# Kernel optimization log

Measured on AMD Instinct MI355X. Metric: run time of the kernel, lower is better.

The kernel has to match this reference:

```python
import jax, jax.numpy as jnp
import numpy as np

B, S, HID = 1, 2048, 4096
NH, NKV, HD = 32, 8, 128
WINDOW = 1024
ROPE_THETA = 1e6
NEG = -1e9


def rotate_half(x):
    x1, x2 = jnp.split(x, 2, axis=-1)
    return jnp.concatenate((-x2, x1), axis=-1)


def setup_inputs() -> dict:
    key = jax.random.key(0)
    ks = jax.random.split(key, 10)
    hidden_states = jax.random.normal(ks[0], (B, S, HID), jnp.float32)
    # rotary tables [max_pos, head_dim]
    inv_freq = 1.0 / (ROPE_THETA ** (jnp.arange(0, HD, 2, dtype=jnp.float32) / HD))
    t = jnp.arange(S, dtype=jnp.float32)
    freqs = jnp.outer(t, inv_freq)                       # [S, HD/2]
    emb = jnp.concatenate((freqs, freqs), axis=-1)       # [S, HD]
    cos, sin = jnp.cos(emb), jnp.sin(emb)
    position_ids = jnp.arange(S, dtype=jnp.int64)[None, :].astype(jnp.int32)
    # sliding-window causal additive mask [B,1,S,S]
    i = jnp.arange(S)[:, None]
    j = jnp.arange(S)[None, :]
    allowed = (j <= i) & (j > i - WINDOW)
    attention_mask = jnp.where(allowed, 0.0, NEG).astype(jnp.float32)[None, None]
    sc = 0.02
    Wq = jax.random.normal(ks[1], (HID, NH * HD), jnp.float32) * sc
    bq = jax.random.normal(ks[2], (NH * HD,), jnp.float32) * sc
    Wk = jax.random.normal(ks[3], (HID, NKV * HD), jnp.float32) * sc
    bk = jax.random.normal(ks[4], (NKV * HD,), jnp.float32) * sc
    Wv = jax.random.normal(ks[5], (HID, NKV * HD), jnp.float32) * sc
    bv = jax.random.normal(ks[6], (NKV * HD,), jnp.float32) * sc
    Wo = jax.random.normal(ks[7], (NH * HD, HID), jnp.float32) * sc
    bo = jax.random.normal(ks[8], (HID,), jnp.float32) * sc
    return dict(hidden_states=hidden_states, attention_mask=attention_mask,
                position_ids=position_ids, cos=cos, sin=sin,
                Wq=Wq, bq=bq, Wk=Wk, bk=bk, Wv=Wv, bv=bv, Wo=Wo, bo=bo)


def reference(hidden_states, attention_mask, position_ids, cos, sin,
              Wq, bq, Wk, bk, Wv, bv, Wo, bo):
    bsz, q_len, _ = hidden_states.shape
    q = (hidden_states @ Wq + bq).reshape(bsz, q_len, NH, HD).transpose(0, 2, 1, 3)
    k = (hidden_states @ Wk + bk).reshape(bsz, q_len, NKV, HD).transpose(0, 2, 1, 3)
    v = (hidden_states @ Wv + bv).reshape(bsz, q_len, NKV, HD).transpose(0, 2, 1, 3)
    # RoPE: cos/sin gathered by position_ids -> [B,1,S,HD]
    c = cos[position_ids][:, None]
    s = sin[position_ids][:, None]
    q = q * c + rotate_half(q) * s
    k = k * c + rotate_half(k) * s
    # GQA repeat_kv: [B,NKV,S,HD] -> [B,NH,S,HD]
    n_rep = NH // NKV
    k = jnp.repeat(k, n_rep, axis=1)
    v = jnp.repeat(v, n_rep, axis=1)
    scores = jnp.einsum('bhqd,bhkd->bhqk', q, k) / np.sqrt(HD).astype(np.float32)
    scores = scores + attention_mask[:, :, :, :k.shape[2]]
    probs = jax.nn.softmax(scores.astype(jnp.float32), axis=-1).astype(q.dtype)
    attn = jnp.einsum('bhqk,bhkd->bhqd', probs, v)
    attn = attn.transpose(0, 2, 1, 3).reshape(bsz, q_len, NH * HD)
    return attn @ Wo + bo
```

## Files before the change

kernel.cpp:

```cpp
#include <hip/hip_runtime.h>
#include <stdint.h>

typedef unsigned short u16;
typedef __attribute__((ext_vector_type(4))) float f32x4;
typedef __attribute__((ext_vector_type(16))) float f32x16;
typedef __attribute__((ext_vector_type(8))) __bf16 bf16x8;
typedef __attribute__((ext_vector_type(4))) u16 u16x4;
typedef __attribute__((ext_vector_type(8))) u16 u16x8;
typedef __attribute__((ext_vector_type(4))) unsigned int u32x4;

#define S_LEN 2048
#define HIDDEN 4096
#define NHEAD 32
#define NKVH 8
#define HD 128
#define WIN 1024

__device__ __forceinline__ float bf2f(u16 u) {
  union { unsigned int i; float f; } x; x.i = ((unsigned int)u) << 16; return x.f;
}
__device__ __forceinline__ u16 f2bf(float f) {
  union { float f; unsigned int i; } x; x.f = f;
  unsigned int r = x.i + 0x7FFFu + ((x.i >> 16) & 1u);
  return (u16)(r >> 16);
}

__device__ __forceinline__ void gload16(const void* g, void* l) {
  __builtin_amdgcn_global_load_lds((const __attribute__((address_space(1))) void*)g,
                                   (__attribute__((address_space(3))) void*)l, 16, 0, 0);
}

__device__ __forceinline__ unsigned int cvtpk_bf16(float a, float b) {
  unsigned int w;
  asm("v_cvt_pk_bf16_f32 %0, %1, %2" : "=v"(w) : "v"(a), "v"(b));
  return w;
}

__global__ __launch_bounds__(256) void conv_bf16_k(const float* __restrict__ in, u16* __restrict__ out) {
  size_t i = ((size_t)blockIdx.x * 256 + threadIdx.x) * 8;
  f32x4 a = *(const f32x4*)(in + i);
  f32x4 b = *(const f32x4*)(in + i + 4);
  u16x8 o;
  o[0] = f2bf(a[0]); o[1] = f2bf(a[1]); o[2] = f2bf(a[2]); o[3] = f2bf(a[3]);
  o[4] = f2bf(b[0]); o[5] = f2bf(b[1]); o[6] = f2bf(b[2]); o[7] = f2bf(b[3]);
  *(u16x8*)(out + i) = o;
}

__global__ __launch_bounds__(256) void concat_bias_k(const float* __restrict__ bq, const float* __restrict__ bk,
                                                     const float* __restrict__ bv, float* __restrict__ o) {
  int i = blockIdx.x * 256 + threadIdx.x;
  float v = (i < 4096) ? bq[i] : (i < 5120 ? bk[i - 4096] : bv[i - 5120]);
  o[i] = v;
}

template <typename TIN>
__global__ __launch_bounds__(256) void transpose_bf16_k(const TIN* __restrict__ in, int istride,
                                                        u16* __restrict__ out, int ostride) {
  __shared__ TIN tile[64][68];
  int r0 = blockIdx.x * 64, c0 = blockIdx.y * 64;
  int t = threadIdx.x;
  int tr = t >> 4;
  int tc = (t & 15) * 4;
#pragma unroll
  for (int i = 0; i < 4; ++i) {
    int r = i * 16 + tr;
    const TIN* src = in + (size_t)(r0 + r) * istride + c0 + tc;
    if constexpr (sizeof(TIN) == 4) {
      *(f32x4*)&tile[r][tc] = *(const f32x4*)src;
    } else {
      *(u16x4*)&tile[r][tc] = *(const u16x4*)src;
    }
  }
  __syncthreads();
#pragma unroll
  for (int i = 0; i < 4; ++i) {
    int rr = i * 16 + tr;
    u16x4 o;
#pragma unroll
    for (int j = 0; j < 4; ++j) {
      if constexpr (sizeof(TIN) == 4) o[j] = f2bf((float)tile[tc + j][rr]);
      else o[j] = (u16)tile[tc + j][rr];
    }
    *(u16x4*)(out + (size_t)(c0 + rr) * ostride + r0 + tc) = o;
  }
}

template <int BM, int BN, typename TOUT>
__global__ __launch_bounds__(512, 4) void gemmp_k(const u16* __restrict__ A, const u16* __restrict__ Bt,
                                                  const float* __restrict__ bias, TOUT* __restrict__ C,
                                                  int M, int N, int K) {
  constexpr int WM = BM / 2;
  constexpr int WN = BN / 4;
  constexpr int MRA = WM / 16;
  constexpr int MRB = WN / 16;
  constexpr int NBH = (BM + BN) / 128;
  __shared__ __align__(16) u16 SA[3][BM * 32];
  __shared__ __align__(16) u16 SB[3][BN * 32];

  int tid = threadIdx.x;
  int w = tid >> 6, l = tid & 63;
  int cl = l & 15, g = l >> 4;
  int wr = w >> 2, wc = w & 3;

  int cpx = gridDim.x >> 3;
  int wg = (blockIdx.x & 7) * cpx + (blockIdx.x >> 3);
  int nbm = M / BM;
  int bm = wg % nbm, bn = wg / nbm;

  int srow = w * 16 + (l >> 2);
  int sk = (((l & 3) ^ ((l >> 3) & 3)) * 8);
  const u16* Ag = A + (size_t)(bm * BM) * K;
  const u16* Bg = Bt + (size_t)(bn * BN) * K;
  int rdchunk = (g ^ ((cl >> 1) & 3)) * 8;

  f32x4 acc[MRA][MRB] = {};

  int NT = K >> 5;

  auto stage = [&](int slot, int tt, int h) {
    if (h < BM / 128) {
      gload16(Ag + (size_t)(h * 128 + srow) * K + tt * 32 + sk,
              (void*)(SA[slot] + (h * 128 + w * 16) * 32));
    } else {
      int hb = h - BM / 128;
      gload16(Bg + (size_t)(hb * 128 + srow) * K + tt * 32 + sk,
              (void*)(SB[slot] + (hb * 128 + w * 16) * 32));
    }
  };

#pragma unroll
  for (int h = 0; h < NBH; ++h) stage(0, 0, h);
#pragma unroll
  for (int h = 0; h < NBH; ++h) stage(1, 1, h);

  int bufc = 0;
  int bufs = 2;
  for (int t = 0; t < NT; ++t) {
    if constexpr (NBH == 3) asm volatile("s_waitcnt vmcnt(3)" ::: "memory");
    else asm volatile("s_waitcnt vmcnt(2)" ::: "memory");
    __builtin_amdgcn_s_barrier();
    asm volatile("" ::: "memory");

    int ts = t + 2; if (ts >= NT) ts -= NT;
#pragma unroll
    for (int h = 0; h < NBH; ++h) stage(bufs, ts, h);

    const u16* sa = SA[bufc];
    const u16* sb = SB[bufc];
    bf16x8 af[MRA], bf[MRB];
#pragma unroll
    for (int mi = 0; mi < MRA; ++mi)
      af[mi] = *(const bf16x8*)(sa + (wr * WM + mi * 16 + cl) * 32 + rdchunk);
#pragma unroll
    for (int ni = 0; ni < MRB; ++ni)
      bf[ni] = *(const bf16x8*)(sb + (wc * WN + ni * 16 + cl) * 32 + rdchunk);
    __builtin_amdgcn_s_setprio(1);
#pragma unroll
    for (int mi = 0; mi < MRA; ++mi)
#pragma unroll
      for (int ni = 0; ni < MRB; ++ni)
        acc[mi][ni] = __builtin_amdgcn_mfma_f32_16x16x32_bf16(af[mi], bf[ni], acc[mi][ni], 0, 0, 0);
    __builtin_amdgcn_s_setprio(0);

    bufc = (bufc == 2) ? 0 : bufc + 1;
    bufs = (bufs == 2) ? 0 : bufs + 1;
  }

  asm volatile("s_waitcnt vmcnt(0)" ::: "memory");

#pragma unroll
  for (int mi = 0; mi < MRA; ++mi) {
    int row0 = bm * BM + wr * WM + mi * 16 + g * 4;
#pragma unroll
    for (int ni = 0; ni < MRB; ++ni) {
      int col = bn * BN + wc * WN + ni * 16 + cl;
      float bb = bias[col];
      f32x4 a = acc[mi][ni];
#pragma unroll
      for (int r = 0; r < 4; ++r) {
        float v = a[r] + bb;
        if constexpr (sizeof(TOUT) == 2) C[(size_t)(row0 + r) * N + col] = f2bf(v);
        else C[(size_t)(row0 + r) * N + col] = v;
      }
    }
  }
}

__global__ __launch_bounds__(256) void rope_scatter_k(const u16* __restrict__ qkv, const int* __restrict__ pos,
                                                      const float* __restrict__ cosT, const float* __restrict__ sinT,
                                                      u16* __restrict__ Q, u16* __restrict__ Kf) {
  int p = blockIdx.x * 256 + threadIdx.x;
  int s = p / 2560;
  int rem = p - s * 2560;
  int hs = rem >> 6;
  int d = rem & 63;
  int ps = pos[s];
  const float* cb = cosT + (size_t)ps * 128;
  const float* sb = sinT + (size_t)ps * 128;
  float c0 = cb[d], c1 = cb[d + 64], s0 = sb[d], s1 = sb[d + 64];
  if (hs < NHEAD) {
    const u16* src = qkv + (size_t)s * 6144 + hs * 128;
    float x0 = bf2f(src[d]), x1 = bf2f(src[d + 64]);
    const float qs = 0.08838834764831845f;
    u16* dst = Q + ((size_t)hs * S_LEN + s) * HD;
    dst[d] = f2bf((x0 * c0 - x1 * s0) * qs);
    dst[d + 64] = f2bf((x1 * c1 + x0 * s1) * qs);
  } else {
    int kh = hs - NHEAD;
    const u16* src = qkv + (size_t)s * 6144 + 4096 + kh * 128;
    float x0 = bf2f(src[d]), x1 = bf2f(src[d + 64]);
    int t = s >> 5, cr = s & 31;
    int ks = d >> 4, hi2 = (d >> 3) & 1, j = d & 7;
    size_t base = ((size_t)(kh * 64 + t) * 8 + ks) * 512 + (size_t)(cr + 32 * hi2) * 8 + j;
    Kf[base] = f2bf(x0 * c0 - x1 * s0);
    Kf[base + 4 * 512] = f2bf(x1 * c1 + x0 * s1);
  }
}

__global__ __launch_bounds__(256) void vfrag_k(const u16* __restrict__ qkv, u16* __restrict__ Vf) {
  __shared__ u16 tile[32][136];
  int bid = blockIdx.x;
  int kh = bid >> 6, t = bid & 63;
  int tid = threadIdx.x;
#pragma unroll
  for (int i = 0; i < 2; ++i) {
    int c = tid + i * 256;
    int r = c >> 4, seg = c & 15;
    *(u16x8*)&tile[r][seg * 8] =
        *(const u16x8*)(qkv + (size_t)(t * 32 + r) * 6144 + 5120 + kh * 128 + seg * 8);
  }
  __syncthreads();
#pragma unroll
  for (int i = 0; i < 2; ++i) {
    int pos = tid + i * 256;
    int dt = pos >> 7, sl = (pos >> 6) & 1, l = pos & 63;
    int c2 = l & 31, h2 = l >> 5;
    u16x8 o;
#pragma unroll
    for (int j = 0; j < 8; ++j) o[j] = tile[sl * 16 + h2 * 8 + j][dt * 32 + c2];
    *(u16x8*)(Vf + ((size_t)(kh * 512 + t * 8 + dt * 2 + sl)) * 512 + (size_t)l * 8) = o;
  }
}

__global__ __launch_bounds__(256, 2) void attn_k(const u16* __restrict__ Q, const u16* __restrict__ Kf,
                                                 const u16* __restrict__ Vf, u16* __restrict__ O) {
  int l = threadIdx.x & 63, w = threadIdx.x >> 6;
  int col = l & 31, hi = l >> 5;
  int bid = blockIdx.x;
  int kh = bid & 7;
  int rest = bid >> 3;
  int h = kh * 4 + (rest & 3);
  int q0 = (rest >> 2) * 128 + w * 32;

  bf16x8 qf[8];
  const u16* qbase = Q + ((size_t)h * S_LEN + q0 + col) * HD + hi * 8;
#pragma unroll
  for (int ks = 0; ks < 8; ++ks) qf[ks] = *(const bf16x8*)(qbase + ks * 16);

  f32x16 ot[4];
#pragma unroll
  for (int dt = 0; dt < 4; ++dt)
#pragma unroll
    for (int r = 0; r < 16; ++r) ot[dt][r] = 0.f;
  float m_r = -3.0e38f, l_r = 0.f;

  const u16* kf0 = Kf + (size_t)kh * 64 * 4096 + (size_t)l * 8;
  const u16* vf0 = Vf + (size_t)kh * 512 * 512 + (size_t)l * 8;

  int jstart = q0 >= WIN ? q0 - WIN : 0;
  for (int j0 = jstart; j0 <= q0; j0 += 32) {
    int t = j0 >> 5;
    const u16* kb = kf0 + (size_t)t * 4096;
    bf16x8 kfr[8];
#pragma unroll
    for (int ks = 0; ks < 8; ++ks) kfr[ks] = *(const bf16x8*)(kb + ks * 512);
    f32x16 s = {};
#pragma unroll
    for (int ks = 0; ks < 8; ++ks)
      s = __builtin_amdgcn_mfma_f32_32x32x16_bf16(kfr[ks], qf[ks], s, 0, 0, 0);
    const u16* vb = vf0 + (size_t)t * 4096;
    bf16x8 vfr[8];
#pragma unroll
    for (int c = 0; c < 8; ++c) vfr[c] = *(const bf16x8*)(vb + c * 512);

    if (j0 + 31 > q0 || j0 < q0 - 992) {
      int q = q0 + col;
#pragma unroll
      for (int r = 0; r < 16; ++r) {
        int kv = j0 + (r & 3) + 8 * (r >> 2) + 4 * hi;
        if (kv > q || kv <= q - WIN) s[r] = -3.0e38f;
      }
    }
    float vm = fmaxf(fmaxf(fmaxf(s[0], s[1]), fmaxf(s[2], s[3])),
                     fmaxf(fmaxf(s[4], s[5]), fmaxf(s[6], s[7])));
    vm = fmaxf(vm, fmaxf(fmaxf(fmaxf(s[8], s[9]), fmaxf(s[10], s[11])),
                         fmaxf(fmaxf(s[12], s[13]), fmaxf(s[14], s[15]))));
    vm = fmaxf(vm, __shfl_xor(vm, 32));
    float mnew = fmaxf(m_r, vm);
    float sc = __expf(m_r - mnew);
    m_r = mnew;
    float rs = 0.f;
#pragma unroll
    for (int r = 0; r < 16; ++r) {
      float pv = __expf(s[r] - mnew);
      s[r] = pv;
      rs += pv;
    }
    rs += __shfl_xor(rs, 32);
    l_r = l_r * sc + rs;
#pragma unroll
    for (int dt = 0; dt < 4; ++dt)
#pragma unroll
      for (int r = 0; r < 16; ++r) ot[dt][r] *= sc;

    bf16x8 pb[2];
#pragma unroll
    for (int sl = 0; sl < 2; ++sl) {
      int b = sl * 8;
      unsigned int a0 = cvtpk_bf16(s[b + 0], s[b + 1]);
      unsigned int c0 = cvtpk_bf16(s[b + 4], s[b + 5]);
      asm("v_permlane32_swap_b32 %0, %1" : "+v"(a0), "+v"(c0));
      unsigned int a1 = cvtpk_bf16(s[b + 2], s[b + 3]);
      unsigned int c1 = cvtpk_bf16(s[b + 6], s[b + 7]);
      asm("v_permlane32_swap_b32 %0, %1" : "+v"(a1), "+v"(c1));
      u32x4 pv = {a0, a1, c0, c1};
      pb[sl] = __builtin_bit_cast(bf16x8, pv);
    }
#pragma unroll
    for (int dt = 0; dt < 4; ++dt) {
      ot[dt] = __builtin_amdgcn_mfma_f32_32x32x16_bf16(vfr[dt * 2 + 0], pb[0], ot[dt], 0, 0, 0);
      ot[dt] = __builtin_amdgcn_mfma_f32_32x32x16_bf16(vfr[dt * 2 + 1], pb[1], ot[dt], 0, 0, 0);
    }
  }

  float inv = 1.0f / l_r;
#pragma unroll
  for (int dt = 0; dt < 4; ++dt) {
#pragma unroll
    for (int g2 = 0; g2 < 4; ++g2) {
      u16x4 o;
#pragma unroll
      for (int i = 0; i < 4; ++i) o[i] = f2bf(ot[dt][g2 * 4 + i] * inv);
      *(u16x4*)(O + (size_t)(q0 + col) * HIDDEN + h * HD + dt * 32 + g2 * 8 + hi * 4) = o;
    }
  }
}

extern "C" void kernel_launch(void* const* d_in, const int* in_sizes, int n_in,
                              void* d_out, int out_size, void* d_ws, size_t ws_size,
                              hipStream_t stream) {
  const float* X = (const float*)d_in[0];
  const int* pos = (const int*)d_in[2];
  const float* cosT = (const float*)d_in[3];
  const float* sinT = (const float*)d_in[4];
  const float* Wq = (const float*)d_in[5];
  const float* bq = (const float*)d_in[6];
  const float* Wk = (const float*)d_in[7];
  const float* bk = (const float*)d_in[8];
  const float* Wv = (const float*)d_in[9];
  const float* bv = (const float*)d_in[10];
  const float* Wo = (const float*)d_in[11];
  const float* bo = (const float*)d_in[12];
  float* out = (float*)d_out;

  const size_t MB = 1ull << 20;
  char* ws = (char*)d_ws;
  u16* WT = (u16*)ws;
  u16* Xb = (u16*)(ws + 48 * MB);
  u16* Qs = Xb;
  u16* QKVr = (u16*)(ws + 64 * MB);
  u16* attnO = QKVr;
  u16* Kfr = (u16*)(ws + 88 * MB);
  u16* Vfr = (u16*)(ws + 92 * MB);
  float* bqkv = (float*)(ws + 96 * MB);

  conv_bf16_k<<<4096, 256, 0, stream>>>(X, Xb);
  transpose_bf16_k<float><<<dim3(64, 64), 256, 0, stream>>>(Wq, 4096, WT, 4096);
  transpose_bf16_k<float><<<dim3(64, 16), 256, 0, stream>>>(Wk, 1024, WT + (size_t)4096 * 4096, 4096);
  transpose_bf16_k<float><<<dim3(64, 16), 256, 0, stream>>>(Wv, 1024, WT + (size_t)5120 * 4096, 4096);
  concat_bias_k<<<24, 256, 0, stream>>>(bq, bk, bv, bqkv);

  gemmp_k<128, 256, u16><<<384, 512, 0, stream>>>(Xb, WT, bqkv, QKVr, 2048, 6144, 4096);

  rope_scatter_k<<<20480, 256, 0, stream>>>(QKVr, pos, cosT, sinT, Qs, Kfr);
  vfrag_k<<<512, 256, 0, stream>>>(QKVr, Vfr);
  transpose_bf16_k<float><<<dim3(64, 64), 256, 0, stream>>>(Wo, 4096, WT, 4096);

  attn_k<<<512, 256, 0, stream>>>(Qs, Kfr, Vfr, attnO);

  gemmp_k<128, 128, float><<<512, 512, 0, stream>>>(attnO, WT, bo, out, 2048, 4096, 4096);
}
```

Before: 346.7 us.

## Rework GEMM with 64-deep K tiles, split staging and retuned tile shapes

Replaces the GEMM kernel with a variant that loads 64-wide K slices per stage using an 8-chunk XOR swizzle. It processes each slice in two halves, interleaving the next stage's global loads between the LDS fragment reads and the MFMAs. The QKV projection now uses 128x192 tiles on 512 blocks, and the output projection uses 128x256 tiles on 256 blocks. The aim is fewer barriers per K element, better load/compute overlap and more operand reuse per tile. In exchange it uses more LDS and registers per block (launch bounds drop to 2 blocks per SM), adds extra barriers inside each iteration, and leaves fewer blocks for the output GEMM.

```diff
diff --git a/kernel.cpp b/kernel.cpp
--- a/kernel.cpp
+++ b/kernel.cpp
@@ -85,17 +85,13 @@
   }
 }
 
-template <int BM, int BN, typename TOUT>
-__global__ __launch_bounds__(512, 4) void gemmp_k(const u16* __restrict__ A, const u16* __restrict__ Bt,
-                                                  const float* __restrict__ bias, TOUT* __restrict__ C,
-                                                  int M, int N, int K) {
-  constexpr int WM = BM / 2;
-  constexpr int WN = BN / 4;
-  constexpr int MRA = WM / 16;
-  constexpr int MRB = WN / 16;
-  constexpr int NBH = (BM + BN) / 128;
-  __shared__ __align__(16) u16 SA[3][BM * 32];
-  __shared__ __align__(16) u16 SB[3][BN * 32];
+template <int BN, int MRB, typename TOUT>
+__global__ __launch_bounds__(512, 2) void gemm2p_k(const u16* __restrict__ A, const u16* __restrict__ Bt,
+                                                   const float* __restrict__ bias, TOUT* __restrict__ C,
+                                                   int M, int N, int K) {
+  constexpr int NL = 2 + BN / 64;
+  __shared__ __align__(16) u16 SA[3][128 * 64];
+  __shared__ __align__(16) u16 SB[3][BN * 64];
 
   int tid = threadIdx.x;
   int w = tid >> 6, l = tid & 63;
@@ -104,76 +100,83 @@
 
   int cpx = gridDim.x >> 3;
   int wg = (blockIdx.x & 7) * cpx + (blockIdx.x >> 3);
-  int nbm = M / BM;
+  int nbm = M >> 7;
   int bm = wg % nbm, bn = wg / nbm;
 
-  int srow = w * 16 + (l >> 2);
-  int sk = (((l & 3) ^ ((l >> 3) & 3)) * 8);
-  const u16* Ag = A + (size_t)(bm * BM) * K;
+  const u16* Ag = A + (size_t)(bm * 128) * K;
   const u16* Bg = Bt + (size_t)(bn * BN) * K;
-  int rdchunk = (g ^ ((cl >> 1) & 3)) * 8;
-
-  f32x4 acc[MRA][MRB] = {};
-
-  int NT = K >> 5;
+  int lr = l >> 3;
+  int csrc = ((l & 7) ^ lr) * 8;
+  int rsw = cl & 7;
+
+  f32x4 acc[4][MRB] = {};
+  int NT = K >> 6;
 
   auto stage = [&](int slot, int tt, int h) {
-    if (h < BM / 128) {
-      gload16(Ag + (size_t)(h * 128 + srow) * K + tt * 32 + sk,
-              (void*)(SA[slot] + (h * 128 + w * 16) * 32));
+    if (h < 2) {
+      int rb = h * 64 + w * 8;
+      gload16(Ag + (size_t)(rb + lr) * K + tt * 64 + csrc, (void*)(SA[slot] + rb * 64));
     } else {
-      int hb = h - BM / 128;
-      gload16(Bg + (size_t)(hb * 128 + srow) * K + tt * 32 + sk,
-              (void*)(SB[slot] + (hb * 128 + w * 16) * 32));
+      int rb = (h - 2) * 64 + w * 8;
+      gload16(Bg + (size_t)(rb + lr) * K + tt * 64 + csrc, (void*)(SB[slot] + rb * 64));
     }
   };
 
 #pragma unroll
-  for (int h = 0; h < NBH; ++h) stage(0, 0, h);
-#pragma unroll
-  for (int h = 0; h < NBH; ++h) stage(1, 1, h);
-
-  int bufc = 0;
-  int bufs = 2;
+  for (int h = 0; h < NL; ++h) stage(0, 0, h);
+#pragma unroll
+  for (int h = 0; h < NL; ++h) stage(1, 1, h);
+
   for (int t = 0; t < NT; ++t) {
-    if constexpr (NBH == 3) asm volatile("s_waitcnt vmcnt(3)" ::: "memory");
-    else asm volatile("s_waitcnt vmcnt(2)" ::: "memory");
+    if constexpr (NL == 5) asm volatile("s_waitcnt vmcnt(5)" ::: "memory");
+    else asm volatile("s_waitcnt vmcnt(6)" ::: "memory");
     __builtin_amdgcn_s_barrier();
     asm volatile("" ::: "memory");
 
+    int slot = t % 3, ss = (t + 2) % 3;
     int ts = t + 2; if (ts >= NT) ts -= NT;
-#pragma unroll
-    for (int h = 0; h < NBH; ++h) stage(bufs, ts, h);
-
-    const u16* sa = SA[bufc];
-    const u16* sb = SB[bufc];
-    bf16x8 af[MRA], bf[MRB];
-#pragma unroll
-    for (int mi = 0; mi < MRA; ++mi)
-      af[mi] = *(const bf16x8*)(sa + (wr * WM + mi * 16 + cl) * 32 + rdchunk);
-#pragma unroll
-    for (int ni = 0; ni < MRB; ++ni)
-      bf[ni] = *(const bf16x8*)(sb + (wc * WN + ni * 16 + cl) * 32 + rdchunk);
-    __builtin_amdgcn_s_setprio(1);
-#pragma unroll
-    for (int mi = 0; mi < MRA; ++mi)
+    const u16* sa = SA[slot];
+    const u16* sb = SB[slot];
+
+#pragma unroll
+    for (int kh = 0; kh < 2; ++kh) {
+      bf16x8 af[4], bf[MRB];
+      int rc = ((kh * 4 + g) ^ rsw) * 8;
+#pragma unroll
+      for (int mi = 0; mi < 4; ++mi)
+        af[mi] = *(const bf16x8*)(sa + (wr * 64 + mi * 16 + cl) * 64 + rc);
 #pragma unroll
       for (int ni = 0; ni < MRB; ++ni)
-        acc[mi][ni] = __builtin_amdgcn_mfma_f32_16x16x32_bf16(af[mi], bf[ni], acc[mi][ni], 0, 0, 0);
-    __builtin_amdgcn_s_setprio(0);
-
-    bufc = (bufc == 2) ? 0 : bufc + 1;
-    bufs = (bufs == 2) ? 0 : bufs + 1;
+        bf[ni] = *(const bf16x8*)(sb + (wc * (MRB * 16) + ni * 16 + cl) * 64 + rc);
+      if (kh == 0) {
+#pragma unroll
+        for (int h = 0; h < (NL + 1) / 2; ++h) stage(ss, ts, h);
+      } else {
+#pragma unroll
+        for (int h = (NL + 1) / 2; h < NL; ++h) stage(ss, ts, h);
+      }
+      __builtin_amdgcn_s_barrier();
+      asm volatile("" ::: "memory");
+      __builtin_amdgcn_s_setprio(1);
+#pragma unroll
+      for (int mi = 0; mi < 4; ++mi)
+#pragma unroll
+        for (int ni = 0; ni < MRB; ++ni)
+          acc[mi][ni] = __builtin_amdgcn_mfma_f32_16x16x32_bf16(af[mi], bf[ni], acc[mi][ni], 0, 0, 0);
+      __builtin_amdgcn_s_setprio(0);
+      __builtin_amdgcn_s_barrier();
+      asm volatile("" ::: "memory");
+    }
   }
 
   asm volatile("s_waitcnt vmcnt(0)" ::: "memory");
 
 #pragma unroll
-  for (int mi = 0; mi < MRA; ++mi) {
-    int row0 = bm * BM + wr * WM + mi * 16 + g * 4;
+  for (int mi = 0; mi < 4; ++mi) {
+    int row0 = bm * 128 + wr * 64 + mi * 16 + g * 4;
 #pragma unroll
     for (int ni = 0; ni < MRB; ++ni) {
-      int col = bn * BN + wc * WN + ni * 16 + cl;
+      int col = bn * BN + wc * (MRB * 16) + ni * 16 + cl;
       float bb = bias[col];
       f32x4 a = acc[mi][ni];
 #pragma unroll
@@ -380,7 +383,7 @@
   transpose_bf16_k<float><<<dim3(64, 16), 256, 0, stream>>>(Wv, 1024, WT + (size_t)5120 * 4096, 4096);
   concat_bias_k<<<24, 256, 0, stream>>>(bq, bk, bv, bqkv);
 
-  gemmp_k<128, 256, u16><<<384, 512, 0, stream>>>(Xb, WT, bqkv, QKVr, 2048, 6144, 4096);
+  gemm2p_k<192, 3, u16><<<512, 512, 0, stream>>>(Xb, WT, bqkv, QKVr, 2048, 6144, 4096);
 
   rope_scatter_k<<<20480, 256, 0, stream>>>(QKVr, pos, cosT, sinT, Qs, Kfr);
   vfrag_k<<<512, 256, 0, stream>>>(QKVr, Vfr);
@@ -388,5 +391,5 @@
 
   attn_k<<<512, 256, 0, stream>>>(Qs, Kfr, Vfr, attnO);
 
-  gemmp_k<128, 128, float><<<512, 512, 0, stream>>>(attnO, WT, bo, out, 2048, 4096, 4096);
-}
+  gemm2p_k<256, 4, float><<<256, 512, 0, stream>>>(attnO, WT, bo, out, 2048, 4096, 4096);
+}
```

Result: no change. 344.7 us (-0.6%).

## Restructure GEMM into split-phase pipeline with larger tiles and interleaved loads

Applied to the files above, without the earlier changes.

The GEMM kernel now splits each K-step into two half-phases. Half of the next tile's global loads are issued between LDS fragment reads and MFMA bursts, with extra barriers between the phases. Both projection GEMMs move to larger tiles (256x256 for QKV, 128x256 for the output projection) with fewer workgroups. The LDS swizzle pattern also changes. The goal is better compute/load overlap and more data reuse per block, at the cost of more barriers, fewer blocks in flight, and grids smaller than the CU count (192/256 blocks).

```diff
diff --git a/kernel.cpp b/kernel.cpp
--- a/kernel.cpp
+++ b/kernel.cpp
@@ -85,17 +85,15 @@
   }
 }
 
-template <int BM, int BN, typename TOUT>
-__global__ __launch_bounds__(512, 4) void gemmp_k(const u16* __restrict__ A, const u16* __restrict__ Bt,
-                                                  const float* __restrict__ bias, TOUT* __restrict__ C,
-                                                  int M, int N, int K) {
+template <int BM, int BN, int MINW, typename TOUT>
+__global__ __launch_bounds__(512, MINW) void gemm3_k(const u16* __restrict__ A, const u16* __restrict__ Bt,
+                                                     const float* __restrict__ bias, TOUT* __restrict__ C,
+                                                     int M, int N, int K) {
   constexpr int WM = BM / 2;
-  constexpr int WN = BN / 4;
   constexpr int MRA = WM / 16;
-  constexpr int MRB = WN / 16;
-  constexpr int NBH = (BM + BN) / 128;
-  __shared__ __align__(16) u16 SA[3][BM * 32];
-  __shared__ __align__(16) u16 SB[3][BN * 32];
+  constexpr int NL = (BM + BN) / 128;
+  __shared__ __align__(16) u16 SA[3 * BM * 32];
+  __shared__ __align__(16) u16 SB[3 * BN * 32];
 
   int tid = threadIdx.x;
   int w = tid >> 6, l = tid & 63;
@@ -107,63 +105,75 @@
   int nbm = M / BM;
   int bm = wg % nbm, bn = wg / nbm;
 
-  int srow = w * 16 + (l >> 2);
-  int sk = (((l & 3) ^ ((l >> 3) & 3)) * 8);
   const u16* Ag = A + (size_t)(bm * BM) * K;
   const u16* Bg = Bt + (size_t)(bn * BN) * K;
-  int rdchunk = (g ^ ((cl >> 1) & 3)) * 8;
-
-  f32x4 acc[MRA][MRB] = {};
-
+  int srow = w * 16 + (l >> 2);
+  int csrc = ((l & 3) ^ ((l >> 2) & 3)) * 8;
+  int rsw = cl & 3;
+
+  f32x4 acc[MRA][4] = {};
   int NT = K >> 5;
 
   auto stage = [&](int slot, int tt, int h) {
     if (h < BM / 128) {
-      gload16(Ag + (size_t)(h * 128 + srow) * K + tt * 32 + sk,
-              (void*)(SA[slot] + (h * 128 + w * 16) * 32));
+      gload16(Ag + (size_t)(h * 128 + srow) * K + tt * 32 + csrc,
+              (void*)(SA + slot * (BM * 32) + h * 4096 + w * 512));
     } else {
       int hb = h - BM / 128;
-      gload16(Bg + (size_t)(hb * 128 + srow) * K + tt * 32 + sk,
-              (void*)(SB[slot] + (hb * 128 + w * 16) * 32));
+      gload16(Bg + (size_t)(hb * 128 + srow) * K + tt * 32 + csrc,
+              (void*)(SB + slot * (BN * 32) + hb * 4096 + w * 512));
     }
   };
 
 #pragma unroll
-  for (int h = 0; h < NBH; ++h) stage(0, 0, h);
-#pragma unroll
-  for (int h = 0; h < NBH; ++h) stage(1, 1, h);
-
-  int bufc = 0;
-  int bufs = 2;
+  for (int h = 0; h < NL; ++h) stage(0, 0, h);
+#pragma unroll
+  for (int h = 0; h < NL; ++h) stage(1, 1, h);
+
   for (int t = 0; t < NT; ++t) {
-    if constexpr (NBH == 3) asm volatile("s_waitcnt vmcnt(3)" ::: "memory");
-    else asm volatile("s_waitcnt vmcnt(2)" ::: "memory");
+    if constexpr (NL == 4) asm volatile("s_waitcnt vmcnt(4)" ::: "memory");
+    else asm volatile("s_waitcnt vmcnt(3)" ::: "memory");
     __builtin_amdgcn_s_barrier();
     asm volatile("" ::: "memory");
 
+    int slot = t % 3, ss = (t + 2) % 3;
     int ts = t + 2; if (ts >= NT) ts -= NT;
-#pragma unroll
-    for (int h = 0; h < NBH; ++h) stage(bufs, ts, h);
-
-    const u16* sa = SA[bufc];
-    const u16* sb = SB[bufc];
-    bf16x8 af[MRA], bf[MRB];
+    const u16* sa = SA + slot * (BM * 32);
+    const u16* sb = SB + slot * (BN * 32);
+
+    bf16x8 af[MRA], b0, b1;
 #pragma unroll
     for (int mi = 0; mi < MRA; ++mi)
-      af[mi] = *(const bf16x8*)(sa + (wr * WM + mi * 16 + cl) * 32 + rdchunk);
-#pragma unroll
-    for (int ni = 0; ni < MRB; ++ni)
-      bf[ni] = *(const bf16x8*)(sb + (wc * WN + ni * 16 + cl) * 32 + rdchunk);
+      af[mi] = *(const bf16x8*)(sa + (wr * WM + mi * 16 + cl) * 32 + ((g ^ rsw) << 3));
+    b0 = *(const bf16x8*)(sb + (wc * 64 + 0 * 16 + cl) * 32 + ((g ^ rsw) << 3));
+    b1 = *(const bf16x8*)(sb + (wc * 64 + 1 * 16 + cl) * 32 + ((g ^ rsw) << 3));
+#pragma unroll
+    for (int h = 0; h < (NL + 1) / 2; ++h) stage(ss, ts, h);
+    __builtin_amdgcn_s_barrier();
+    asm volatile("" ::: "memory");
     __builtin_amdgcn_s_setprio(1);
 #pragma unroll
-    for (int mi = 0; mi < MRA; ++mi)
-#pragma unroll
-      for (int ni = 0; ni < MRB; ++ni)
-        acc[mi][ni] = __builtin_amdgcn_mfma_f32_16x16x32_bf16(af[mi], bf[ni], acc[mi][ni], 0, 0, 0);
+    for (int mi = 0; mi < MRA; ++mi) {
+      acc[mi][0] = __builtin_amdgcn_mfma_f32_16x16x32_bf16(af[mi], b0, acc[mi][0], 0, 0, 0);
+      acc[mi][1] = __builtin_amdgcn_mfma_f32_16x16x32_bf16(af[mi], b1, acc[mi][1], 0, 0, 0);
+    }
     __builtin_amdgcn_s_setprio(0);
-
-    bufc = (bufc == 2) ? 0 : bufc + 1;
-    bufs = (bufs == 2) ? 0 : bufs + 1;
+    __builtin_amdgcn_s_barrier();
+    asm volatile("" ::: "memory");
+
+    b0 = *(const bf16x8*)(sb + (wc * 64 + 2 * 16 + cl) * 32 + ((g ^ rsw) << 3));
+    b1 = *(const bf16x8*)(sb + (wc * 64 + 3 * 16 + cl) * 32 + ((g ^ rsw) << 3));
+#pragma unroll
+    for (int h = (NL + 1) / 2; h < NL; ++h) stage(ss, ts, h);
+    __builtin_amdgcn_s_barrier();
+    asm volatile("" ::: "memory");
+    __builtin_amdgcn_s_setprio(1);
+#pragma unroll
+    for (int mi = 0; mi < MRA; ++mi) {
+      acc[mi][2] = __builtin_amdgcn_mfma_f32_16x16x32_bf16(af[mi], b0, acc[mi][2], 0, 0, 0);
+      acc[mi][3] = __builtin_amdgcn_mfma_f32_16x16x32_bf16(af[mi], b1, acc[mi][3], 0, 0, 0);
+    }
+    __builtin_amdgcn_s_setprio(0);
   }
 
   asm volatile("s_waitcnt vmcnt(0)" ::: "memory");
@@ -172,8 +182,8 @@
   for (int mi = 0; mi < MRA; ++mi) {
     int row0 = bm * BM + wr * WM + mi * 16 + g * 4;
 #pragma unroll
-    for (int ni = 0; ni < MRB; ++ni) {
-      int col = bn * BN + wc * WN + ni * 16 + cl;
+    for (int ni = 0; ni < 4; ++ni) {
+      int col = bn * BN + wc * 64 + ni * 16 + cl;
       float bb = bias[col];
       f32x4 a = acc[mi][ni];
 #pragma unroll
@@ -380,7 +390,7 @@
   transpose_bf16_k<float><<<dim3(64, 16), 256, 0, stream>>>(Wv, 1024, WT + (size_t)5120 * 4096, 4096);
   concat_bias_k<<<24, 256, 0, stream>>>(bq, bk, bv, bqkv);
 
-  gemmp_k<128, 256, u16><<<384, 512, 0, stream>>>(Xb, WT, bqkv, QKVr, 2048, 6144, 4096);
+  gemm3_k<256, 256, 2, u16><<<192, 512, 0, stream>>>(Xb, WT, bqkv, QKVr, 2048, 6144, 4096);
 
   rope_scatter_k<<<20480, 256, 0, stream>>>(QKVr, pos, cosT, sinT, Qs, Kfr);
   vfrag_k<<<512, 256, 0, stream>>>(QKVr, Vfr);
@@ -388,5 +398,5 @@
 
   attn_k<<<512, 256, 0, stream>>>(Qs, Kfr, Vfr, attnO);
 
-  gemmp_k<128, 128, float><<<512, 512, 0, stream>>>(attnO, WT, bo, out, 2048, 4096, 4096);
-}
+  gemm3_k<128, 256, 4, float><<<256, 512, 0, stream>>>(attnO, WT, bo, out, 2048, 4096, 4096);
+}
```

Result: slower. 357.6 us (+3.2%).

## Rework GEMM kernel to 4-wave 2x2 blocks with 128x192 QKV tiles

Applied to the files above, without the earlier changes.

Replaces the 8-wave (2x4) GEMM with a 4-wave (2x2) variant. Each wave now computes a larger sub-tile, and each thread issues more global-to-LDS loads per stage. The QKV projection moves from 128x256 tiles on 384 blocks to 128x192 tiles on 512 blocks, which fills the CUs more evenly. The aim is better register reuse per wave and better grid balance, at the cost of fewer waves to hide latency and more accumulator registers per thread.

```diff
diff --git a/kernel.cpp b/kernel.cpp
--- a/kernel.cpp
+++ b/kernel.cpp
@@ -85,75 +85,72 @@
   }
 }
 
-template <int BM, int BN, typename TOUT>
-__global__ __launch_bounds__(512, 4) void gemmp_k(const u16* __restrict__ A, const u16* __restrict__ Bt,
-                                                  const float* __restrict__ bias, TOUT* __restrict__ C,
-                                                  int M, int N, int K) {
-  constexpr int WM = BM / 2;
-  constexpr int WN = BN / 4;
-  constexpr int MRA = WM / 16;
-  constexpr int MRB = WN / 16;
-  constexpr int NBH = (BM + BN) / 128;
-  __shared__ __align__(16) u16 SA[3][BM * 32];
-  __shared__ __align__(16) u16 SB[3][BN * 32];
+template <int BM, int BN, int MINW, typename TOUT>
+__global__ __launch_bounds__(256, MINW) void gemm4_k(const u16* __restrict__ A, const u16* __restrict__ Bt,
+                                                     const float* __restrict__ bias, TOUT* __restrict__ C,
+                                                     int M, int N, int K) {
+  constexpr int WM = BM / 2, WN = BN / 2;
+  constexpr int MRA = WM / 16, MRB = WN / 16;
+  constexpr int NA = BM / 64, NB = BN / 64;
+  constexpr int NL = NA + NB;
+  __shared__ __align__(16) u16 SA[3 * BM * 32];
+  __shared__ __align__(16) u16 SB[3 * BN * 32];
 
   int tid = threadIdx.x;
   int w = tid >> 6, l = tid & 63;
   int cl = l & 15, g = l >> 4;
-  int wr = w >> 2, wc = w & 3;
+  int wr = w >> 1, wc = w & 1;
 
   int cpx = gridDim.x >> 3;
   int wg = (blockIdx.x & 7) * cpx + (blockIdx.x >> 3);
   int nbm = M / BM;
   int bm = wg % nbm, bn = wg / nbm;
 
-  int srow = w * 16 + (l >> 2);
-  int sk = (((l & 3) ^ ((l >> 3) & 3)) * 8);
   const u16* Ag = A + (size_t)(bm * BM) * K;
   const u16* Bg = Bt + (size_t)(bn * BN) * K;
-  int rdchunk = (g ^ ((cl >> 1) & 3)) * 8;
+  int srow = w * 16 + (l >> 2);
+  int csrc = ((l & 3) ^ ((l >> 3) & 3)) * 8;
+  int rdc = (g ^ ((cl >> 1) & 3)) << 3;
 
   f32x4 acc[MRA][MRB] = {};
-
   int NT = K >> 5;
 
   auto stage = [&](int slot, int tt, int h) {
-    if (h < BM / 128) {
-      gload16(Ag + (size_t)(h * 128 + srow) * K + tt * 32 + sk,
-              (void*)(SA[slot] + (h * 128 + w * 16) * 32));
+    if (h < NA) {
+      gload16(Ag + (size_t)(h * 64 + srow) * K + tt * 32 + csrc,
+              (void*)(SA + slot * (BM * 32) + (h * 64 + w * 16) * 32));
     } else {
-      int hb = h - BM / 128;
-      gload16(Bg + (size_t)(hb * 128 + srow) * K + tt * 32 + sk,
-              (void*)(SB[slot] + (hb * 128 + w * 16) * 32));
+      int hb = h - NA;
+      gload16(Bg + (size_t)(hb * 64 + srow) * K + tt * 32 + csrc,
+              (void*)(SB + slot * (BN * 32) + (hb * 64 + w * 16) * 32));
     }
   };
 
 #pragma unroll
-  for (int h = 0; h < NBH; ++h) stage(0, 0, h);
-#pragma unroll
-  for (int h = 0; h < NBH; ++h) stage(1, 1, h);
-
-  int bufc = 0;
-  int bufs = 2;
+  for (int h = 0; h < NL; ++h) stage(0, 0, h);
+#pragma unroll
+  for (int h = 0; h < NL; ++h) stage(1, 1, h);
+
   for (int t = 0; t < NT; ++t) {
-    if constexpr (NBH == 3) asm volatile("s_waitcnt vmcnt(3)" ::: "memory");
-    else asm volatile("s_waitcnt vmcnt(2)" ::: "memory");
+    if constexpr (NL == 5) asm volatile("s_waitcnt vmcnt(5)" ::: "memory");
+    else asm volatile("s_waitcnt vmcnt(4)" ::: "memory");
     __builtin_amdgcn_s_barrier();
     asm volatile("" ::: "memory");
 
+    int slot = t % 3, ss = (t + 2) % 3;
     int ts = t + 2; if (ts >= NT) ts -= NT;
 #pragma unroll
-    for (int h = 0; h < NBH; ++h) stage(bufs, ts, h);
-
-    const u16* sa = SA[bufc];
-    const u16* sb = SB[bufc];
+    for (int h = 0; h < NL; ++h) stage(ss, ts, h);
+
+    const u16* sa = SA + slot * (BM * 32);
+    const u16* sb = SB + slot * (BN * 32);
     bf16x8 af[MRA], bf[MRB];
 #pragma unroll
     for (int mi = 0; mi < MRA; ++mi)
-      af[mi] = *(const bf16x8*)(sa + (wr * WM + mi * 16 + cl) * 32 + rdchunk);
+      af[mi] = *(const bf16x8*)(sa + (wr * WM + mi * 16 + cl) * 32 + rdc);
 #pragma unroll
     for (int ni = 0; ni < MRB; ++ni)
-      bf[ni] = *(const bf16x8*)(sb + (wc * WN + ni * 16 + cl) * 32 + rdchunk);
+      bf[ni] = *(const bf16x8*)(sb + (wc * WN + ni * 16 + cl) * 32 + rdc);
     __builtin_amdgcn_s_setprio(1);
 #pragma unroll
     for (int mi = 0; mi < MRA; ++mi)
@@ -161,9 +158,6 @@
       for (int ni = 0; ni < MRB; ++ni)
         acc[mi][ni] = __builtin_amdgcn_mfma_f32_16x16x32_bf16(af[mi], bf[ni], acc[mi][ni], 0, 0, 0);
     __builtin_amdgcn_s_setprio(0);
-
-    bufc = (bufc == 2) ? 0 : bufc + 1;
-    bufs = (bufs == 2) ? 0 : bufs + 1;
   }
 
   asm volatile("s_waitcnt vmcnt(0)" ::: "memory");
@@ -380,7 +374,7 @@
   transpose_bf16_k<float><<<dim3(64, 16), 256, 0, stream>>>(Wv, 1024, WT + (size_t)5120 * 4096, 4096);
   concat_bias_k<<<24, 256, 0, stream>>>(bq, bk, bv, bqkv);
 
-  gemmp_k<128, 256, u16><<<384, 512, 0, stream>>>(Xb, WT, bqkv, QKVr, 2048, 6144, 4096);
+  gemm4_k<128, 192, 2, u16><<<512, 256, 0, stream>>>(Xb, WT, bqkv, QKVr, 2048, 6144, 4096);
 
   rope_scatter_k<<<20480, 256, 0, stream>>>(QKVr, pos, cosT, sinT, Qs, Kfr);
   vfrag_k<<<512, 256, 0, stream>>>(QKVr, Vfr);
@@ -388,5 +382,5 @@
 
   attn_k<<<512, 256, 0, stream>>>(Qs, Kfr, Vfr, attnO);
 
-  gemmp_k<128, 128, float><<<512, 512, 0, stream>>>(attnO, WT, bo, out, 2048, 4096, 4096);
-}
+  gemm4_k<128, 128, 2, float><<<512, 256, 0, stream>>>(attnO, WT, bo, out, 2048, 4096, 4096);
+}
```

New measurement: 348.4 us. No clear change (+0.5%).
